# Optimization experiments

Measured on AMD Instinct MI355X. Metric: run time of the kernel, lower is better.

The kernel has to match this reference:

```python
import jax, jax.numpy as jnp
import numpy as np

NR, NL, K, TOPK, C, B = 4096, 16384, 8, 10, 16, 4
W_OCC, W_MDN, W_INT = 0.2, 1.0, 0.1
LOG2PI = float(np.log(2.0 * np.pi))


def setup_inputs() -> dict:
    key = jax.random.key(0)
    ks = jax.random.split(key, 12)
    radar_indices = jnp.concatenate([
        jax.random.randint(ks[0], (NR, 1), 0, B),
        jax.random.randint(ks[1], (NR, 1), 0, 41),
        jax.random.randint(ks[2], (NR, 2), 0, 176),
    ], axis=1).astype(jnp.int32)
    lidar_indices = jnp.concatenate([
        jax.random.randint(ks[3], (NL, 1), 0, B),
        jax.random.randint(ks[4], (NL, 1), 0, 41),
        jax.random.randint(ks[5], (NL, 2), 0, 176),
    ], axis=1).astype(jnp.int32)
    return {
        'mu_off': jax.random.normal(ks[6], (NR, K, 3)) * 2.0,
        'log_sig_off': jax.random.normal(ks[7], (NR, K, 3)) * 0.3,
        'mu_int': jax.random.normal(ks[8], (NR, K, 1)),
        'occ_logit': jax.random.normal(ks[9], (NR, K, 1)),
        'mix_logit': jax.random.normal(ks[10], (NR, K, 1)),
        'lidar_features': jax.random.normal(ks[11], (NL, C)),
        'radar_indices': radar_indices,
        'lidar_indices': lidar_indices,
        'gt_topk': TOPK,
    }


def _match(radar_indices, lidar_indices, topk):
    # per-batch top-k nearest lidar voxels for each radar voxel (vectorized:
    # dense masked distance matrix replaces the per-batch python loop)
    rb, lb = radar_indices[:, 0], lidar_indices[:, 0]
    rpos = radar_indices[:, 1:].astype(jnp.float32)  # (Nr,3) zyx
    lpos = lidar_indices[:, 1:].astype(jnp.float32)  # (Nl,3)
    d2 = ((rpos * rpos).sum(-1)[:, None] + (lpos * lpos).sum(-1)[None, :]
          - 2.0 * (rpos @ lpos.T))  # (Nr,Nl) squared dist, same order as cdist
    same = rb[:, None] == lb[None, :]
    d2 = jnp.where(same, d2, jnp.inf)  # cross-batch pairs excluded
    _, nn_idx = jax.lax.top_k(-d2, topk)  # (Nr,topk) smallest distances
    matched = same.any(axis=1)  # (Nr,)
    offs_zyx = (lidar_indices[nn_idx, 1:]
                - radar_indices[:, None, 1:]).astype(jnp.float32)  # (Nr,topk,3)
    offs_zyx = jnp.where(matched[:, None, None], offs_zyx, 0.0)
    return matched, nn_idx, offs_zyx


def reference(mu_off, log_sig_off, mu_int, occ_logit, mix_logit,
              lidar_features, radar_indices, lidar_indices, gt_topk):
    matched, nn_idx, offs_zyx = _match(radar_indices, lidar_indices, gt_topk)
    gt_feat = jnp.where(matched[:, None, None], lidar_features[nn_idx], 0.0)  # (Nr,T,C)
    y = offs_zyx[..., ::-1]  # flip zyx -> xyz, (Nr,T,3)

    # occupancy BCE-with-logits against matched mask
    occ_any = occ_logit[..., 0].max(axis=1)  # (Nr,)
    tgt = matched.astype(occ_any.dtype)
    occ_loss = (tgt * jax.nn.softplus(-occ_any)
                + (1.0 - tgt) * jax.nn.softplus(occ_any)).mean()

    # MDN log-prob: (Nr,T,K) mixture components
    log_pi = jax.nn.log_softmax(mix_logit[..., 0], axis=1)  # (Nr,K)
    mu_ = mu_off[:, None, :, :]       # (Nr,1,K,3)
    ls_ = log_sig_off[:, None, :, :]
    sigma2 = jnp.exp(2.0 * ls_) + 1e-12
    y_ = y[:, :, None, :]             # (Nr,T,1,3)
    logN = -0.5 * (((y_ - mu_) ** 2) / sigma2 + 2.0 * ls_ + LOG2PI).sum(-1)  # (Nr,T,K)
    log_post = logN + log_pi[:, None, :]
    logp = jax.nn.logsumexp(log_post, axis=-1)  # (Nr,T)

    # masked means emulate boolean-index-then-mean over matched rows
    m = matched.astype(jnp.float32)
    cnt = m.sum()
    T = logp.shape[1]
    mdn_nll = -(logp * m[:, None]).sum() / (cnt * T)

    # intensity loss (C % 4 == 0 path)
    gt_int = gt_feat.reshape(gt_feat.shape[0], gt_feat.shape[1], C // 4, 4)[..., 3].mean(axis=2)  # (Nr,T)
    r = jax.nn.softmax(log_post, axis=-1)  # (Nr,T,K) responsibilities
    term = r * jnp.abs(mu_int[:, None, :, 0] - gt_int[:, :, None])  # (Nr,T,K)
    int_loss = (term * m[:, None, None]).sum() / (cnt * T * r.shape[-1])

    return W_OCC * occ_loss + W_MDN * mdn_nll + W_INT * int_loss
```

## Files before the change

kernel.cpp:

```cpp
#include <hip/hip_runtime.h>
#include <cstdint>

#define NRAD 4096
#define NLID 16384
#define KMIX 8
#define TOPK 10
#define CF   16
#define NBIN 176
#define YWIN 13
#define LOG2PI 1.8378770664093453f

static constexpr unsigned INF_D2 = 62851u;

__device__ __forceinline__ void insert_key(unsigned (&t)[TOPK], unsigned key) {
#pragma unroll
    for (int i = TOPK - 1; i >= 1; --i) {
        unsigned hi = key > t[i - 1] ? key : t[i - 1];
        t[i] = hi < t[i] ? hi : t[i];
    }
    t[0] = key < t[0] ? key : t[0];
}

__device__ __forceinline__ void merge10(unsigned (&t)[TOPK], int lane,
                                        unsigned& mine, unsigned& first, unsigned& tenth) {
#pragma unroll
    for (int r = 0; r < TOPK; ++r) {
        unsigned v = t[0];
#pragma unroll
        for (int off = 32; off >= 1; off >>= 1) {
            unsigned o = __shfl_xor(v, off, 64);
            v = o < v ? o : v;
        }
        if (t[0] == v) {
#pragma unroll
            for (int i = 0; i < TOPK - 1; ++i) t[i] = t[i + 1];
            t[TOPK - 1] = 0xFFFFFFFFu;
        }
        if (lane == r) mine = v;
        if (r == 0) first = v;
        if (r == TOPK - 1) tenth = v;
    }
}

__device__ __forceinline__ float waveReduceSum(float v) {
#pragma unroll
    for (int off = 32; off >= 1; off >>= 1) v += __shfl_down(v, off, 64);
    return v;
}

__device__ __forceinline__ void scan_range(unsigned (&t)[TOPK], const uint2* __restrict__ base,
                                           int s, int e, int rz, int ry, int rx, int lane) {
    for (int i = s + lane; i < e; i += 64) {
        uint2 c = base[i];
        int dz = (int)((c.x >> 16) & 63u)  - rz;
        int dy = (int)((c.x >> 8)  & 255u) - ry;
        int dx = (int)(c.x & 255u)         - rx;
        unsigned d2 = (unsigned)(__mul24(dz, dz) + __mul24(dy, dy) + __mul24(dx, dx));
        unsigned key = (d2 << 14) | c.y;
        if (key < t[TOPK - 1]) insert_key(t, key);
    }
}

__global__ __launch_bounds__(1024) void prep_kernel(
        const int* __restrict__ lidar_indices,
        unsigned* __restrict__ packed_full,
        uint2* __restrict__ compacted,
        int* __restrict__ binoff_g,
        int* __restrict__ ctrl) {
    __shared__ int hist[NBIN];
    __shared__ int binoff_s[NBIN + 1];
    __shared__ int bcur[NBIN];
    int tid = threadIdx.x, myb = blockIdx.x;
    if (tid < NBIN) hist[tid] = 0;

    int4 li[NLID / 1024];
#pragma unroll
    for (int it = 0; it < NLID / 1024; ++it)
        li[it] = ((const int4*)lidar_indices)[it * 1024 + tid];
    __syncthreads();

#pragma unroll
    for (int it = 0; it < NLID / 1024; ++it)
        if (li[it].x == myb) atomicAdd(&hist[li[it].z], 1);
    __syncthreads();

    if (tid < 64) {
        int carry = 0;
#pragma unroll
        for (int c = 0; c < 3; ++c) {
            int idx = c * 64 + tid;
            int h = (idx < NBIN) ? hist[idx] : 0;
            int v = h;
#pragma unroll
            for (int off = 1; off < 64; off <<= 1) {
                int u = __shfl_up(v, off, 64);
                if (tid >= off) v += u;
            }
            if (idx < NBIN) binoff_s[idx] = carry + v - h;
            carry += __shfl(v, 63, 64);
        }
        if (tid == 0) binoff_s[NBIN] = carry;
    }
    __syncthreads();
    if (tid < NBIN) bcur[tid] = binoff_s[tid];
    __syncthreads();

#pragma unroll
    for (int it = 0; it < NLID / 1024; ++it) {
        int i = it * 1024 + tid;
        unsigned pos = ((unsigned)li[it].y << 16) | ((unsigned)li[it].z << 8) | (unsigned)li[it].w;
        if (li[it].x == myb) {
            packed_full[i] = ((unsigned)li[it].x << 22) | pos;
            int dst = atomicAdd(&bcur[li[it].z], 1);
            compacted[myb * NLID + dst] = make_uint2(pos, (unsigned)i);
        }
    }

    __syncthreads();
    if (tid <= NBIN) binoff_g[myb * (NBIN + 1) + tid] = binoff_s[tid];
    if (myb == 0 && tid >= 64 && tid < 69) ctrl[4 + (tid - 64)] = 0;
}

__global__ __launch_bounds__(256) void topk_kernel(
        const uint2* __restrict__ compacted,
        const unsigned* __restrict__ packed_full,
        const int* __restrict__ binoff_g,
        const int* __restrict__ radar_indices,
        int* __restrict__ nn_out, int* __restrict__ matched_out) {
    int lane = threadIdx.x & 63;
    int row  = blockIdx.x * 4 + (threadIdx.x >> 6);
    int4 ri = ((const int4*)radar_indices)[row];
    int rb = ri.x, rz = ri.y, ry = ri.z, rx = ri.w;
    const int* boff = binoff_g + rb * (NBIN + 1);

    int lo = ry - YWIN;      lo = lo < 0 ? 0 : lo;
    int hi = ry + YWIN + 1;  hi = hi > NBIN ? NBIN : hi;
    int s = boff[lo], e = boff[hi];

    unsigned t[TOPK];
#pragma unroll
    for (int i = 0; i < TOPK; ++i) t[i] = 0xFFFFFFFFu;

    const uint2* base = compacted + rb * NLID;
    int s0 = s & ~1;
    const uint4* src4 = (const uint4*)(base + s0);
    int iters = (e - s0 + 127) >> 7;
    uint4 q = src4[lane];
    for (int it = 0; it < iters; ++it) {
        uint4 qn = q;
        if (it + 1 < iters) qn = src4[(it + 1) * 64 + lane];
        int p = s0 + (it * 64 + lane) * 2;
        {
            int dz = (int)((q.x >> 16) & 63u)  - rz;
            int dy = (int)((q.x >> 8)  & 255u) - ry;
            int dx = (int)(q.x & 255u)         - rx;
            unsigned d2 = (unsigned)(__mul24(dz, dz) + __mul24(dy, dy) + __mul24(dx, dx));
            unsigned key = (p >= s && p < e) ? ((d2 << 14) | q.y) : 0xFFFFFFFFu;
            if (key < t[TOPK - 1]) insert_key(t, key);
        }
        {
            int dz = (int)((q.z >> 16) & 63u)  - rz;
            int dy = (int)((q.z >> 8)  & 255u) - ry;
            int dx = (int)(q.z & 255u)         - rx;
            unsigned d2 = (unsigned)(__mul24(dz, dz) + __mul24(dy, dy) + __mul24(dx, dx));
            unsigned key = (p + 1 < e) ? ((d2 << 14) | q.w) : 0xFFFFFFFFu;
            if (key < t[TOPK - 1]) insert_key(t, key);
        }
        q = qn;
    }

    unsigned mine = 0xFFFFFFFFu, first = 0, tenth = 0;
    merge10(t, lane, mine, first, tenth);
    bool matched = true;

    unsigned lim = 0xFFFFFFFFu;
    if (lo > 0)    { unsigned d = (unsigned)(ry - lo + 1); unsigned v = d * d; lim = v < lim ? v : lim; }
    if (hi < NBIN) { unsigned d = (unsigned)(hi - ry);     unsigned v = d * d; lim = v < lim ? v : lim; }

    if ((tenth >> 14) >= lim) {
#pragma unroll
        for (int i = 0; i < TOPK; ++i) t[i] = 0xFFFFFFFFu;
        t[0] = mine;
        scan_range(t, base, boff[0], s, rz, ry, rx, lane);
        scan_range(t, base, e, boff[NBIN], rz, ry, rx, lane);
        merge10(t, lane, mine, first, tenth);
    }

    if (tenth == 0xFFFFFFFFu) {
#pragma unroll
        for (int i = 0; i < TOPK; ++i) t[i] = 0xFFFFFFFFu;
        for (int it = 0; it < NLID / 256; ++it) {
            uint4 p4 = ((const uint4*)packed_full)[it * 64 + lane];
            unsigned bse = it * 256 + lane * 4;
            unsigned ps[4] = {p4.x, p4.y, p4.z, p4.w};
#pragma unroll
            for (int j = 0; j < 4; ++j) {
                unsigned p = ps[j];
                int b  = (int)(p >> 22);
                int dz = (int)((p >> 16) & 63u)  - rz;
                int dy = (int)((p >> 8)  & 255u) - ry;
                int dx = (int)(p & 255u)         - rx;
                unsigned d2 = (unsigned)(__mul24(dz, dz) + __mul24(dy, dy) + __mul24(dx, dx));
                unsigned hi2 = (b == rb) ? d2 : INF_D2;
                insert_key(t, (hi2 << 14) | (bse + j));
            }
        }
        merge10(t, lane, mine, first, tenth);
        matched = first < (INF_D2 << 14);
    }

    if (lane < TOPK) nn_out[row * TOPK + lane] = (int)(mine & 0x3FFFu);
    if (lane == 0)   matched_out[row] = matched ? 1 : 0;
}

__global__ __launch_bounds__(256) void mdn_kernel(
        const float* __restrict__ mu_off, const float* __restrict__ log_sig_off,
        const float* __restrict__ mu_int, const float* __restrict__ occ_logit,
        const float* __restrict__ mix_logit, const float* __restrict__ lidar_features,
        const int* __restrict__ radar_indices, const int* __restrict__ lidar_indices,
        const int* __restrict__ nn, const int* __restrict__ matched,
        float* __restrict__ accum,
        unsigned* __restrict__ dctr,
        float* __restrict__ out) {
    int gid = blockIdx.x * 256 + threadIdx.x;
    int n  = gid / TOPK;
    int tt = gid - n * TOPK;
    int m  = matched[n];
    float mf = (float)m;
    int nni = nn[gid];

    int4 ri = ((const int4*)radar_indices)[n];
    int4 li = ((const int4*)lidar_indices)[nni];
    float y0 = mf * (float)(li.w - ri.w);
    float y1 = mf * (float)(li.z - ri.z);
    float y2 = mf * (float)(li.y - ri.y);

    float mix[KMIX];
    float mmax = -1e30f;
#pragma unroll
    for (int k = 0; k < KMIX; ++k) {
        mix[k] = mix_logit[n * KMIX + k];
        mmax = fmaxf(mmax, mix[k]);
    }
    float msum = 0.f;
#pragma unroll
    for (int k = 0; k < KMIX; ++k) msum += expf(mix[k] - mmax);
    float logZ = mmax + logf(msum);

    float lpost[KMIX];
    float pmax = -1e30f;
#pragma unroll
    for (int k = 0; k < KMIX; ++k) {
        int bidx = (n * KMIX + k) * 3;
        float mu0 = mu_off[bidx + 0], mu1 = mu_off[bidx + 1], mu2 = mu_off[bidx + 2];
        float l0 = log_sig_off[bidx + 0], l1 = log_sig_off[bidx + 1], l2 = log_sig_off[bidx + 2];
        float s0 = expf(2.f * l0) + 1e-12f;
        float s1 = expf(2.f * l1) + 1e-12f;
        float s2 = expf(2.f * l2) + 1e-12f;
        float d0 = y0 - mu0, d1 = y1 - mu1, d2v = y2 - mu2;
        float q = d0 * d0 / s0 + d1 * d1 / s1 + d2v * d2v / s2
                + 2.f * (l0 + l1 + l2) + 3.f * LOG2PI;
        lpost[k] = -0.5f * q + (mix[k] - logZ);
        pmax = fmaxf(pmax, lpost[k]);
    }
    float ex[KMIX];
    float se = 0.f;
#pragma unroll
    for (int k = 0; k < KMIX; ++k) { ex[k] = expf(lpost[k] - pmax); se += ex[k]; }
    float logp = pmax + logf(se);

    float gt = 0.f;
    if (m) {
        const float* lf = lidar_features + nni * CF;
        gt = 0.25f * (lf[3] + lf[7] + lf[11] + lf[15]);
    }
    float inv_se = 1.f / se;
    float isum = 0.f;
#pragma unroll
    for (int k = 0; k < KMIX; ++k)
        isum += ex[k] * inv_se * fabsf(mu_int[n * KMIX + k] - gt);

    float lp = mf * logp;
    float ip = mf * isum;
    float oc = 0.f, mc = 0.f;
    if (tt == 0) {
        float oa = -1e30f;
#pragma unroll
        for (int k = 0; k < KMIX; ++k) oa = fmaxf(oa, occ_logit[n * KMIX + k]);
        float soft_abs = log1pf(expf(-fabsf(oa)));
        oc = mf * (soft_abs + fmaxf(-oa, 0.f)) + (1.f - mf) * (soft_abs + fmaxf(oa, 0.f));
        mc = mf;
    }

    lp = waveReduceSum(lp); ip = waveReduceSum(ip);
    oc = waveReduceSum(oc); mc = waveReduceSum(mc);
    __shared__ float sA[4], sB[4], sC[4], sD[4];
    int wid = threadIdx.x >> 6, lane = threadIdx.x & 63;
    if (lane == 0) { sA[wid] = lp; sB[wid] = ip; sC[wid] = oc; sD[wid] = mc; }
    __syncthreads();
    if (threadIdx.x == 0) {
        atomicAdd(&accum[0], sA[0] + sA[1] + sA[2] + sA[3]);
        atomicAdd(&accum[1], sB[0] + sB[1] + sB[2] + sB[3]);
        atomicAdd(&accum[2], sC[0] + sC[1] + sC[2] + sC[3]);
        atomicAdd(&accum[3], sD[0] + sD[1] + sD[2] + sD[3]);
        __threadfence();
        unsigned done = atomicAdd(dctr, 1u);
        if (done == gridDim.x - 1) {
            __threadfence();
            float a = __hip_atomic_load(&accum[0], __ATOMIC_RELAXED, __HIP_MEMORY_SCOPE_AGENT);
            float b = __hip_atomic_load(&accum[1], __ATOMIC_RELAXED, __HIP_MEMORY_SCOPE_AGENT);
            float c = __hip_atomic_load(&accum[2], __ATOMIC_RELAXED, __HIP_MEMORY_SCOPE_AGENT);
            float d = __hip_atomic_load(&accum[3], __ATOMIC_RELAXED, __HIP_MEMORY_SCOPE_AGENT);
            float occ_loss = c / (float)NRAD;
            float mdn_nll  = -a / (d * (float)TOPK);
            float int_loss = b / (d * (float)TOPK * (float)KMIX);
            out[0] = 0.2f * occ_loss + mdn_nll + 0.1f * int_loss;
        }
    }
}

extern "C" void kernel_launch(void* const* d_in, const int* in_sizes, int n_in,
                              void* d_out, int out_size, void* d_ws, size_t ws_size,
                              hipStream_t stream) {
    const float* mu_off         = (const float*)d_in[0];
    const float* log_sig_off    = (const float*)d_in[1];
    const float* mu_int         = (const float*)d_in[2];
    const float* occ_logit      = (const float*)d_in[3];
    const float* mix_logit      = (const float*)d_in[4];
    const float* lidar_features = (const float*)d_in[5];
    const int*   radar_indices  = (const int*)d_in[6];
    const int*   lidar_indices  = (const int*)d_in[7];
    float* out = (float*)d_out;

    char* ws = (char*)d_ws;
    unsigned* packed_full = (unsigned*)(ws + 0);
    uint2*    compacted   = (uint2*)(ws + 65536);
    int*      ctrl        = (int*)(ws + 589824);
    int*      nn          = (int*)(ws + 589888);
    int*      matched     = (int*)(ws + 753728);
    int*      binoff_g    = (int*)(ws + 770112);

    float*    accum = (float*)(ctrl + 4);
    unsigned* dctr  = (unsigned*)(ctrl + 8);

    hipLaunchKernelGGL(prep_kernel, dim3(4), dim3(1024), 0, stream,
                       lidar_indices, packed_full, compacted, binoff_g, ctrl);
    hipLaunchKernelGGL(topk_kernel, dim3(NRAD / 4), dim3(256), 0, stream,
                       compacted, packed_full, binoff_g, radar_indices, nn, matched);
    hipLaunchKernelGGL(mdn_kernel, dim3(NRAD * TOPK / 256), dim3(256), 0, stream,
                       mu_off, log_sig_off, mu_int, occ_logit, mix_logit,
                       lidar_features, radar_indices, lidar_indices,
                       nn, matched, accum, dctr, out);
}
```

Measured before the change: 112.6 us.

## Fuse top-k matching and MDN loss kernels into one launch

Merges the top-k neighbour search and the MDN/intensity/occupancy loss computation into a single kernel. Each block stores its four rows' neighbour indices and match flags in shared memory, then wave 0 computes the 40 (row, neighbour) terms and atomically accumulates them. This removes one kernel launch and the global round trip for nn/matched. The accumulators are spread across separate cache lines, but there are now 1024 blocks each issuing atomics. Only one wave per block does the loss work while the others exit, and that wave runs 24 of its 64 lanes idle.

Measured after the change: 129.9 us. 1.15x slower.

```diff
diff --git a/kernel.cpp b/kernel.cpp
--- a/kernel.cpp
+++ b/kernel.cpp
@@ -66,7 +66,8 @@
         unsigned* __restrict__ packed_full,
         uint2* __restrict__ compacted,
         int* __restrict__ binoff_g,
-        int* __restrict__ ctrl) {
+        float* __restrict__ accum,
+        unsigned* __restrict__ dctr) {
     __shared__ int hist[NBIN];
     __shared__ int binoff_s[NBIN + 1];
     __shared__ int bcur[NBIN];
@@ -118,17 +119,27 @@
 
     __syncthreads();
     if (tid <= NBIN) binoff_g[myb * (NBIN + 1) + tid] = binoff_s[tid];
-    if (myb == 0 && tid >= 64 && tid < 69) ctrl[4 + (tid - 64)] = 0;
-}
-
-__global__ __launch_bounds__(256) void topk_kernel(
+    if (myb == 0) {
+        if (tid >= 64 && tid < 68) accum[(tid - 64) * 16] = 0.f;
+        if (tid == 68) *dctr = 0u;
+    }
+}
+
+__global__ __launch_bounds__(256) void topk_mdn_kernel(
         const uint2* __restrict__ compacted,
         const unsigned* __restrict__ packed_full,
         const int* __restrict__ binoff_g,
         const int* __restrict__ radar_indices,
-        int* __restrict__ nn_out, int* __restrict__ matched_out) {
+        const int* __restrict__ lidar_indices,
+        const float* __restrict__ mu_off, const float* __restrict__ log_sig_off,
+        const float* __restrict__ mu_int, const float* __restrict__ occ_logit,
+        const float* __restrict__ mix_logit, const float* __restrict__ lidar_features,
+        float* __restrict__ accum,
+        unsigned* __restrict__ dctr,
+        float* __restrict__ out) {
     int lane = threadIdx.x & 63;
-    int row  = blockIdx.x * 4 + (threadIdx.x >> 6);
+    int wid  = threadIdx.x >> 6;
+    int row  = blockIdx.x * 4 + wid;
     int4 ri = ((const int4*)radar_indices)[row];
     int rb = ri.x, rz = ri.y, ry = ri.z, rx = ri.w;
     const int* boff = binoff_g + rb * (NBIN + 1);
@@ -209,31 +220,26 @@
         matched = first < (INF_D2 << 14);
     }
 
-    if (lane < TOPK) nn_out[row * TOPK + lane] = (int)(mine & 0x3FFFu);
-    if (lane == 0)   matched_out[row] = matched ? 1 : 0;
-}
-
-__global__ __launch_bounds__(256) void mdn_kernel(
-        const float* __restrict__ mu_off, const float* __restrict__ log_sig_off,
-        const float* __restrict__ mu_int, const float* __restrict__ occ_logit,
-        const float* __restrict__ mix_logit, const float* __restrict__ lidar_features,
-        const int* __restrict__ radar_indices, const int* __restrict__ lidar_indices,
-        const int* __restrict__ nn, const int* __restrict__ matched,
-        float* __restrict__ accum,
-        unsigned* __restrict__ dctr,
-        float* __restrict__ out) {
-    int gid = blockIdx.x * 256 + threadIdx.x;
-    int n  = gid / TOPK;
-    int tt = gid - n * TOPK;
-    int m  = matched[n];
-    float mf = (float)m;
-    int nni = nn[gid];
-
-    int4 ri = ((const int4*)radar_indices)[n];
+    __shared__ int   s_nn[4][TOPK];
+    __shared__ int   s_row[4];
+    __shared__ float s_mf[4];
+    if (lane < TOPK) s_nn[wid][lane] = (int)(mine & 0x3FFFu);
+    if (lane == 0) { s_row[wid] = row; s_mf[wid] = matched ? 1.f : 0.f; }
+    __syncthreads();
+    if (wid != 0) return;
+
+    bool act = lane < 4 * TOPK;
+    int w  = lane / TOPK;
+    int tt = lane - w * TOPK;
+    int n   = act ? s_row[w] : 0;
+    float mf = act ? s_mf[w] : 0.f;
+    int nni = act ? s_nn[w][tt] : 0;
+
+    int4 rr = ((const int4*)radar_indices)[n];
     int4 li = ((const int4*)lidar_indices)[nni];
-    float y0 = mf * (float)(li.w - ri.w);
-    float y1 = mf * (float)(li.z - ri.z);
-    float y2 = mf * (float)(li.y - ri.y);
+    float y0 = mf * (float)(li.w - rr.w);
+    float y1 = mf * (float)(li.z - rr.z);
+    float y2 = mf * (float)(li.y - rr.y);
 
     float mix[KMIX];
     float mmax = -1e30f;
@@ -258,9 +264,9 @@
         float s1 = expf(2.f * l1) + 1e-12f;
         float s2 = expf(2.f * l2) + 1e-12f;
         float d0 = y0 - mu0, d1 = y1 - mu1, d2v = y2 - mu2;
-        float q = d0 * d0 / s0 + d1 * d1 / s1 + d2v * d2v / s2
-                + 2.f * (l0 + l1 + l2) + 3.f * LOG2PI;
-        lpost[k] = -0.5f * q + (mix[k] - logZ);
+        float qv = d0 * d0 / s0 + d1 * d1 / s1 + d2v * d2v / s2
+                 + 2.f * (l0 + l1 + l2) + 3.f * LOG2PI;
+        lpost[k] = -0.5f * qv + (mix[k] - logZ);
         pmax = fmaxf(pmax, lpost[k]);
     }
     float ex[KMIX];
@@ -270,7 +276,7 @@
     float logp = pmax + logf(se);
 
     float gt = 0.f;
-    if (m) {
+    if (act && mf != 0.f) {
         const float* lf = lidar_features + nni * CF;
         gt = 0.25f * (lf[3] + lf[7] + lf[11] + lf[15]);
     }
@@ -280,10 +286,10 @@
     for (int k = 0; k < KMIX; ++k)
         isum += ex[k] * inv_se * fabsf(mu_int[n * KMIX + k] - gt);
 
-    float lp = mf * logp;
-    float ip = mf * isum;
+    float lp = act ? mf * logp : 0.f;
+    float ip = act ? mf * isum : 0.f;
     float oc = 0.f, mc = 0.f;
-    if (tt == 0) {
+    if (act && tt == 0) {
         float oa = -1e30f;
 #pragma unroll
         for (int k = 0; k < KMIX; ++k) oa = fmaxf(oa, occ_logit[n * KMIX + k]);
@@ -294,23 +300,19 @@
 
     lp = waveReduceSum(lp); ip = waveReduceSum(ip);
     oc = waveReduceSum(oc); mc = waveReduceSum(mc);
-    __shared__ float sA[4], sB[4], sC[4], sD[4];
-    int wid = threadIdx.x >> 6, lane = threadIdx.x & 63;
-    if (lane == 0) { sA[wid] = lp; sB[wid] = ip; sC[wid] = oc; sD[wid] = mc; }
-    __syncthreads();
-    if (threadIdx.x == 0) {
-        atomicAdd(&accum[0], sA[0] + sA[1] + sA[2] + sA[3]);
-        atomicAdd(&accum[1], sB[0] + sB[1] + sB[2] + sB[3]);
-        atomicAdd(&accum[2], sC[0] + sC[1] + sC[2] + sC[3]);
-        atomicAdd(&accum[3], sD[0] + sD[1] + sD[2] + sD[3]);
+    if (lane == 0) {
+        atomicAdd(&accum[0],  lp);
+        atomicAdd(&accum[16], ip);
+        atomicAdd(&accum[32], oc);
+        atomicAdd(&accum[48], mc);
         __threadfence();
         unsigned done = atomicAdd(dctr, 1u);
         if (done == gridDim.x - 1) {
             __threadfence();
-            float a = __hip_atomic_load(&accum[0], __ATOMIC_RELAXED, __HIP_MEMORY_SCOPE_AGENT);
-            float b = __hip_atomic_load(&accum[1], __ATOMIC_RELAXED, __HIP_MEMORY_SCOPE_AGENT);
-            float c = __hip_atomic_load(&accum[2], __ATOMIC_RELAXED, __HIP_MEMORY_SCOPE_AGENT);
-            float d = __hip_atomic_load(&accum[3], __ATOMIC_RELAXED, __HIP_MEMORY_SCOPE_AGENT);
+            float a = __hip_atomic_load(&accum[0],  __ATOMIC_RELAXED, __HIP_MEMORY_SCOPE_AGENT);
+            float b = __hip_atomic_load(&accum[16], __ATOMIC_RELAXED, __HIP_MEMORY_SCOPE_AGENT);
+            float c = __hip_atomic_load(&accum[32], __ATOMIC_RELAXED, __HIP_MEMORY_SCOPE_AGENT);
+            float d = __hip_atomic_load(&accum[48], __ATOMIC_RELAXED, __HIP_MEMORY_SCOPE_AGENT);
             float occ_loss = c / (float)NRAD;
             float mdn_nll  = -a / (d * (float)TOPK);
             float int_loss = b / (d * (float)TOPK * (float)KMIX);
@@ -335,20 +337,14 @@
     char* ws = (char*)d_ws;
     unsigned* packed_full = (unsigned*)(ws + 0);
     uint2*    compacted   = (uint2*)(ws + 65536);
-    int*      ctrl        = (int*)(ws + 589824);
-    int*      nn          = (int*)(ws + 589888);
-    int*      matched     = (int*)(ws + 753728);
-    int*      binoff_g    = (int*)(ws + 770112);
-
-    float*    accum = (float*)(ctrl + 4);
-    unsigned* dctr  = (unsigned*)(ctrl + 8);
+    int*      binoff_g    = (int*)(ws + 589824);
+    float*    accum       = (float*)(ws + 593920);
+    unsigned* dctr        = (unsigned*)(ws + 594176);
 
     hipLaunchKernelGGL(prep_kernel, dim3(4), dim3(1024), 0, stream,
-                       lidar_indices, packed_full, compacted, binoff_g, ctrl);
-    hipLaunchKernelGGL(topk_kernel, dim3(NRAD / 4), dim3(256), 0, stream,
-                       compacted, packed_full, binoff_g, radar_indices, nn, matched);
-    hipLaunchKernelGGL(mdn_kernel, dim3(NRAD * TOPK / 256), dim3(256), 0, stream,
+                       lidar_indices, packed_full, compacted, binoff_g, accum, dctr);
+    hipLaunchKernelGGL(topk_mdn_kernel, dim3(NRAD / 4), dim3(256), 0, stream,
+                       compacted, packed_full, binoff_g, radar_indices, lidar_indices,
                        mu_off, log_sig_off, mu_int, occ_logit, mix_logit,
-                       lidar_features, radar_indices, lidar_indices,
-                       nn, matched, accum, dctr, out);
-}
+                       lidar_features, accum, dctr, out);
+}
```
